# Optimization experiments

Measured on AMD Instinct MI355X. Metric: run time of the kernel, lower is better.

Reference implementation:

```python
import jax, jax.numpy as jnp
import numpy as np

INPUT_DIM = 784
LATENT_DIM = 32
HIDDEN = 256
NUM_PROTO = 25  # 5x5 SOM grid
BATCH = 65536


def setup_inputs() -> dict:
    key = jax.random.key(0)
    ks = jax.random.split(key, 10)
    s = lambda fan_in: 1.0 / np.sqrt(fan_in)
    return {
        "x": jax.random.uniform(ks[0], (BATCH, INPUT_DIM), dtype=jnp.float32),
        # encoder: Linear(784,256) -> ReLU -> Linear(256,32)
        "We1": jax.random.normal(ks[1], (INPUT_DIM, HIDDEN), dtype=jnp.float32) * s(INPUT_DIM),
        "be1": jnp.zeros((HIDDEN,), dtype=jnp.float32),
        "We2": jax.random.normal(ks[2], (HIDDEN, LATENT_DIM), dtype=jnp.float32) * s(HIDDEN),
        "be2": jnp.zeros((LATENT_DIM,), dtype=jnp.float32),
        # decoder: Linear(32,256) -> ReLU -> Linear(256,784) -> Sigmoid
        "Wd1": jax.random.normal(ks[3], (LATENT_DIM, HIDDEN), dtype=jnp.float32) * s(LATENT_DIM),
        "bd1": jnp.zeros((HIDDEN,), dtype=jnp.float32),
        "Wd2": jax.random.normal(ks[4], (HIDDEN, INPUT_DIM), dtype=jnp.float32) * s(HIDDEN),
        "bd2": jnp.zeros((INPUT_DIM,), dtype=jnp.float32),
        # SOM prototypes (torch.randn init)
        "prototypes": jax.random.normal(ks[5], (NUM_PROTO, LATENT_DIM), dtype=jnp.float32),
    }


def reference(x, We1, be1, We2, be2, Wd1, bd1, Wd2, bd2, prototypes):
    # encoder
    h = jax.nn.relu(x @ We1 + be1)          # [B, 256]
    z = h @ We2 + be2                        # [B, 32]
    # SOM layer: cdist -> argmin -> gather winning prototype
    # squared euclidean distance suffices for argmin
    sq_dists = (jnp.sum(z * z, axis=1, keepdims=True)
                - 2.0 * (z @ prototypes.T)
                + jnp.sum(prototypes * prototypes, axis=1))  # [B, 25]
    min_idx = jnp.argmin(sq_dists, axis=1)   # [B]
    som_z = prototypes[min_idx]              # [B, 32]
    # decoder
    hd = jax.nn.relu(som_z @ Wd1 + bd1)      # [B, 256]
    x_recon = jax.nn.sigmoid(hd @ Wd2 + bd2)  # [B, 784]
    return (x_recon, z, som_z)
```

## Files before the change

### kernel.cpp

```cpp
#include <hip/hip_runtime.h>
#include <hip/hip_bf16.h>
#include <math.h>

#define BATCH   65536
#define IN_DIM  784
#define HID     256
#define LAT     32
#define NPROTO  25

typedef short  short8  __attribute__((ext_vector_type(8)));
typedef float  floatx4 __attribute__((ext_vector_type(4)));

__device__ __forceinline__ unsigned short f2bf(float v) {
    __hip_bfloat16 b = __float2bfloat16(v);
    return *reinterpret_cast<unsigned short*>(&b);
}
__device__ __forceinline__ float bf2f(unsigned short u) {
    __hip_bfloat16 b = *reinterpret_cast<__hip_bfloat16*>(&u);
    return __bfloat162float(b);
}
__device__ __forceinline__ void split3(float v, unsigned short& o1,
                                       unsigned short& o2, unsigned short& o3) {
    o1 = f2bf(v); float r1 = v - bf2f(o1);
    o2 = f2bf(r1); float r2 = r1 - bf2f(o2);
    o3 = f2bf(r2);
}

__device__ __forceinline__ floatx4 mm_bf16(short8 a, short8 b, floatx4 c) {
    return __builtin_amdgcn_mfma_f32_16x16x32_bf16(a, b, c, 0, 0, 0);
}

#define BT_SHORTS  204800
#define WS_NEEDED  1307200

__global__ __launch_bounds__(256)
void prep_BF(const float* __restrict__ We1,
             unsigned short* __restrict__ B1,
             unsigned short* __restrict__ B2,
             unsigned short* __restrict__ B3)
{
    int t   = blockIdx.x * 256 + threadIdx.x;
    int l15 = t & 15;
    int q   = (t >> 4) & 3;
    int sn  = t >> 6;
    int s   = sn >> 4;
    int n   = (sn & 15) * 16 + l15;
    int k0  = s * 32 + q * 8;
    short8 v1, v2, v3;
#pragma unroll
    for (int j = 0; j < 8; ++j) {
        int k = k0 + j;
        float v = (k < IN_DIM) ? We1[(size_t)k * HID + n] : 0.f;
        unsigned short a, b, c;
        split3(v, a, b, c);
        v1[j] = (short)a;
        v2[j] = (short)b;
        v3[j] = (short)c;
    }
    size_t o = (size_t)t * 8;
    *(short8*)(B1 + o) = v1;
    *(short8*)(B2 + o) = v2;
    *(short8*)(B3 + o) = v3;
}

__global__ __launch_bounds__(256)
void dpsom_dectab(const float* __restrict__ protos,
                  const float* __restrict__ Wd1,
                  const float* __restrict__ bd1,
                  const float* __restrict__ Wd2,
                  const float* __restrict__ bd2,
                  float* __restrict__ table)
{
    __shared__ float pr[LAT];
    __shared__ float hd[HID];
    const int p = blockIdx.x;
    const int tid = threadIdx.x;
    if (tid < LAT) pr[tid] = protos[p * LAT + tid];
    __syncthreads();
    float s = bd1[tid];
#pragma unroll
    for (int k = 0; k < LAT; ++k)
        s = fmaf(pr[k], Wd1[k * HID + tid], s);
    hd[tid] = fmaxf(s, 0.f);
    __syncthreads();
    for (int i = tid; i < IN_DIM; i += 256) {
        float o = bd2[i];
        for (int j = 0; j < HID; ++j)
            o = fmaf(hd[j], Wd2[(size_t)j * IN_DIM + i], o);
        table[p * IN_DIM + i] = 1.f / (1.f + expf(-o));
    }
}

#define AST  80
#define ABUF 15360

__device__ __forceinline__ void cvt_write3(float4 v0, float4 v1, char* wp) {
    float vv[8] = {v0.x, v0.y, v0.z, v0.w, v1.x, v1.y, v1.z, v1.w};
    short8 u1, u2, u3;
#pragma unroll
    for (int j = 0; j < 8; ++j) {
        unsigned short a, b, c;
        split3(vv[j], a, b, c);
        u1[j] = (short)a;
        u2[j] = (short)b;
        u3[j] = (short)c;
    }
    *(short8*)(wp)          = u1;
    *(short8*)(wp + 5120)   = u2;
    *(short8*)(wp + 10240)  = u3;
}

__global__ __launch_bounds__(256, 3)
void dpsom_encoder_bf3(const float* __restrict__ x,
                       const unsigned short* __restrict__ B1g,
                       const unsigned short* __restrict__ B2g,
                       const unsigned short* __restrict__ B3g,
                       const float* __restrict__ be1,
                       const float* __restrict__ We2,
                       const float* __restrict__ be2,
                       const float* __restrict__ protos,
                       const float* __restrict__ table,
                       float* __restrict__ z_out,
                       float* __restrict__ somz_out,
                       float* __restrict__ xrec)
{
    __shared__ __align__(16) char smem[45056];
    const int tid  = threadIdx.x;
    const int wave = tid >> 6;
    const int lane = tid & 63;
    const int l15  = lane & 15;
    const int q    = lane >> 4;
    const int row0 = blockIdx.x * 64;

    const int arow = tid >> 2;
    const int aq   = tid & 3;
    const float* xrow = x + (size_t)(row0 + arow) * IN_DIM + aq * 8;
    char* awp = smem + arow * AST + aq * 16;

    floatx4 acc[4][4];
#pragma unroll
    for (int i = 0; i < 4; ++i)
#pragma unroll
        for (int j = 0; j < 4; ++j) acc[i][j] = (floatx4)0.f;

    {
        float4 v0 = *(const float4*)(xrow);
        float4 v1 = *(const float4*)(xrow + 4);
        cvt_write3(v0, v1, awp);
    }
    __syncthreads();

    for (int s = 0; s < 25; ++s) {
        const char* abase = smem + (s & 1) * ABUF;
        const int fb = (s * 16 + wave * 4) << 9;

        short8 b1, b2, b3;
        {
            int off0 = fb + (lane << 3);
            b1 = *(const short8*)(B1g + off0);
            b2 = *(const short8*)(B2g + off0);
            b3 = *(const short8*)(B3g + off0);
        }

        float4 v0 = make_float4(0.f, 0.f, 0.f, 0.f), v1 = v0;
        if (s < 24) {
            if ((s < 23) | (aq < 2)) {
                v0 = *(const float4*)(xrow + (s + 1) * 32);
                v1 = *(const float4*)(xrow + (s + 1) * 32 + 4);
            }
        }

        short8 a1f[4], a2f[4], a3f[4];
#pragma unroll
        for (int mf = 0; mf < 4; ++mf) {
            const char* ap = abase + (mf * 16 + l15) * AST + q * 16;
            a1f[mf] = *(const short8*)ap;
            a2f[mf] = *(const short8*)(ap + 5120);
            a3f[mf] = *(const short8*)(ap + 10240);
        }

        if (s < 24) cvt_write3(v0, v1, awp + ((s + 1) & 1) * ABUF);

#pragma unroll
        for (int nf = 0; nf < 4; ++nf) {
            short8 cb1 = b1, cb2 = b2, cb3 = b3;
            if (nf < 3) {
                int offn = fb + ((nf + 1) << 9) + (lane << 3);
                b1 = *(const short8*)(B1g + offn);
                b2 = *(const short8*)(B2g + offn);
                b3 = *(const short8*)(B3g + offn);
            }
#pragma unroll
            for (int mf = 0; mf < 4; ++mf) acc[mf][nf] = mm_bf16(a1f[mf], cb1, acc[mf][nf]);
#pragma unroll
            for (int mf = 0; mf < 4; ++mf) acc[mf][nf] = mm_bf16(a1f[mf], cb2, acc[mf][nf]);
#pragma unroll
            for (int mf = 0; mf < 4; ++mf) acc[mf][nf] = mm_bf16(a2f[mf], cb1, acc[mf][nf]);
#pragma unroll
            for (int mf = 0; mf < 4; ++mf) acc[mf][nf] = mm_bf16(a1f[mf], cb3, acc[mf][nf]);
#pragma unroll
            for (int mf = 0; mf < 4; ++mf) acc[mf][nf] = mm_bf16(a3f[mf], cb1, acc[mf][nf]);
#pragma unroll
            for (int mf = 0; mf < 4; ++mf) acc[mf][nf] = mm_bf16(a2f[mf], cb2, acc[mf][nf]);
        }
        __syncthreads();
    }

    {
        float bias[4];
#pragma unroll
        for (int nf = 0; nf < 4; ++nf) bias[nf] = be1[wave * 64 + 16 * nf + l15];
#pragma unroll
        for (int mf = 0; mf < 4; ++mf)
#pragma unroll
            for (int nf = 0; nf < 4; ++nf)
#pragma unroll
                for (int r = 0; r < 4; ++r)
                    acc[mf][nf][r] = fmaxf(acc[mf][nf][r] + bias[nf], 0.f);
    }

    float* h_lds  = (float*)smem;
    float* z_lds  = (float*)(smem + 33280);
    float* cdist  = (float*)(smem + 41728);
    int*   cidx   = (int*)  (smem + 42752);
    int*   minidx = (int*)  (smem + 43776);

    const int jz = tid & 31;
    const int rg = tid >> 5;
    const float bz = be2[jz];

    for (int hf = 0; hf < 2; ++hf) {
        __syncthreads();
#pragma unroll
        for (int mm = 0; mm < 2; ++mm) {
            int mf = 2 * hf + mm;
#pragma unroll
            for (int nf = 0; nf < 4; ++nf)
#pragma unroll
                for (int r = 0; r < 4; ++r) {
                    int lr = 16 * mm + 4 * q + r;
                    h_lds[lr * 260 + wave * 64 + 16 * nf + l15] = acc[mf][nf][r];
                }
        }
        __syncthreads();
        float s0 = bz, s1 = bz, s2 = bz, s3 = bz;
        const float* h0p = h_lds + (rg * 4 + 0) * 260;
        const float* h1p = h_lds + (rg * 4 + 1) * 260;
        const float* h2p = h_lds + (rg * 4 + 2) * 260;
        const float* h3p = h_lds + (rg * 4 + 3) * 260;
#pragma unroll 4
        for (int c = 0; c < HID; c += 4) {
            float w0 = We2[(c + 0) * LAT + jz];
            float w1 = We2[(c + 1) * LAT + jz];
            float w2 = We2[(c + 2) * LAT + jz];
            float w3 = We2[(c + 3) * LAT + jz];
            float4 h0 = *(const float4*)(h0p + c);
            float4 h1 = *(const float4*)(h1p + c);
            float4 h2 = *(const float4*)(h2p + c);
            float4 h3 = *(const float4*)(h3p + c);
            s0 = fmaf(h0.x, w0, fmaf(h0.y, w1, fmaf(h0.z, w2, fmaf(h0.w, w3, s0))));
            s1 = fmaf(h1.x, w0, fmaf(h1.y, w1, fmaf(h1.z, w2, fmaf(h1.w, w3, s1))));
            s2 = fmaf(h2.x, w0, fmaf(h2.y, w1, fmaf(h2.z, w2, fmaf(h2.w, w3, s2))));
            s3 = fmaf(h3.x, w0, fmaf(h3.y, w1, fmaf(h3.z, w2, fmaf(h3.w, w3, s3))));
        }
        int rbase = hf * 32 + rg * 4;
        z_lds[(rbase + 0) * 33 + jz] = s0;
        z_lds[(rbase + 1) * 33 + jz] = s1;
        z_lds[(rbase + 2) * 33 + jz] = s2;
        z_lds[(rbase + 3) * 33 + jz] = s3;
        z_out[(size_t)(row0 + rbase + 0) * LAT + jz] = s0;
        z_out[(size_t)(row0 + rbase + 1) * LAT + jz] = s1;
        z_out[(size_t)(row0 + rbase + 2) * LAT + jz] = s2;
        z_out[(size_t)(row0 + rbase + 3) * LAT + jz] = s3;
    }
    __syncthreads();

    {
        const int r = tid & 63;
        const int g = tid >> 6;
        float zr[LAT];
        float zn = 0.f;
#pragma unroll
        for (int j = 0; j < LAT; ++j) {
            zr[j] = z_lds[r * 33 + j];
            zn = fmaf(zr[j], zr[j], zn);
        }
        const int p0 = (g == 0) ? 0 : (1 + g * 6);
        const int pc = (g == 0) ? 7 : 6;
        float best = 3.4e38f;
        int bp = p0;
        for (int pi = 0; pi < pc; ++pi) {
            int p = p0 + pi;
            float dot = 0.f, pn = 0.f;
#pragma unroll
            for (int j = 0; j < LAT; ++j) {
                float pv = protos[p * LAT + j];
                dot = fmaf(zr[j], pv, dot);
                pn  = fmaf(pv, pv, pn);
            }
            float d = zn - 2.f * dot + pn;
            if (d < best) { best = d; bp = p; }
        }
        cdist[r * 4 + g] = best;
        cidx[r * 4 + g]  = bp;
    }
    __syncthreads();
    if (tid < 64) {
        float best = cdist[tid * 4];
        int bp = cidx[tid * 4];
#pragma unroll
        for (int g = 1; g < 4; ++g) {
            float d = cdist[tid * 4 + g];
            if (d < best) { best = d; bp = cidx[tid * 4 + g]; }
        }
        minidx[tid] = bp;
    }
    __syncthreads();

#pragma unroll
    for (int m = 0; m < 8; ++m) {
        int r = rg * 8 + m;
        somz_out[(size_t)(row0 + r) * LAT + jz] = protos[minidx[r] * LAT + jz];
    }

    for (int i2 = tid; i2 < 64 * 196; i2 += 256) {
        int row = i2 / 196;
        int c   = i2 - row * 196;
        int idx = minidx[row];
        ((float4*)xrec)[(size_t)(row0 + row) * 196 + c] =
            ((const float4*)table)[idx * 196 + c];
    }
}

#define BMf 64
#define BKf 16
#define HSTRIDE 260
#define ZSTRIDE 33
#define SMEM_FLOATS 10432

__global__ __launch_bounds__(256)
void dpsom_encoder_fp32(const float* __restrict__ x,
                        const float* __restrict__ We1,
                        const float* __restrict__ be1,
                        const float* __restrict__ We2,
                        const float* __restrict__ be2,
                        const float* __restrict__ protos,
                        float* __restrict__ z_out,
                        float* __restrict__ somz_out,
                        int* __restrict__ minidx_out)
{
    __shared__ float smem[SMEM_FLOATS];
    __shared__ int minidx_lds[BMf];
    float* As = smem;
    float* Bs = smem + BKf * BMf;
    float* h_lds = smem;
    float* z_lds = smem + 32 * HSTRIDE;

    const int tid = threadIdx.x;
    const int tx = tid & 31;
    const int ty = tid >> 5;
    const int row0 = blockIdx.x * BMf;

    float acc[8][8];
#pragma unroll
    for (int i = 0; i < 8; ++i)
#pragma unroll
        for (int j = 0; j < 8; ++j) acc[i][j] = 0.f;

    const int ar  = tid >> 2;
    const int akq = tid & 3;

    for (int k0 = 0; k0 < IN_DIM; k0 += BKf) {
        __syncthreads();
        float4 av = *(const float4*)(x + (size_t)(row0 + ar) * IN_DIM + k0 + akq * 4);
        As[(akq * 4 + 0) * BMf + ar] = av.x;
        As[(akq * 4 + 1) * BMf + ar] = av.y;
        As[(akq * 4 + 2) * BMf + ar] = av.z;
        As[(akq * 4 + 3) * BMf + ar] = av.w;
#pragma unroll
        for (int i = 0; i < 4; ++i) {
            int f  = tid + i * 256;
            int bk = f >> 6;
            int bn = (f & 63) << 2;
            *(float4*)(Bs + bk * HID + bn) =
                *(const float4*)(We1 + (size_t)(k0 + bk) * HID + bn);
        }
        __syncthreads();
#pragma unroll
        for (int kk = 0; kk < BKf; ++kk) {
            float4 a0 = *(const float4*)(As + kk * BMf + ty * 8);
            float4 a1 = *(const float4*)(As + kk * BMf + ty * 8 + 4);
            float4 b0 = *(const float4*)(Bs + kk * HID + tx * 8);
            float4 b1 = *(const float4*)(Bs + kk * HID + tx * 8 + 4);
            float a[8] = {a0.x, a0.y, a0.z, a0.w, a1.x, a1.y, a1.z, a1.w};
            float b[8] = {b0.x, b0.y, b0.z, b0.w, b1.x, b1.y, b1.z, b1.w};
#pragma unroll
            for (int i = 0; i < 8; ++i)
#pragma unroll
                for (int j = 0; j < 8; ++j)
                    acc[i][j] = fmaf(a[i], b[j], acc[i][j]);
        }
    }
    {
        float bias[8];
#pragma unroll
        for (int j = 0; j < 8; ++j) bias[j] = be1[tx * 8 + j];
#pragma unroll
        for (int i = 0; i < 8; ++i)
#pragma unroll
            for (int j = 0; j < 8; ++j)
                acc[i][j] = fmaxf(acc[i][j] + bias[j], 0.f);
    }
    const int jz = tid & 31;
    const int rg = tid >> 5;
    const float bz = be2[jz];
    for (int hf = 0; hf < 2; ++hf) {
        __syncthreads();
        if ((ty >> 2) == hf) {
            int rb = (ty & 3) * 8;
#pragma unroll
            for (int i = 0; i < 8; ++i) {
                *(float4*)(h_lds + (rb + i) * HSTRIDE + tx * 8) =
                    make_float4(acc[i][0], acc[i][1], acc[i][2], acc[i][3]);
                *(float4*)(h_lds + (rb + i) * HSTRIDE + tx * 8 + 4) =
                    make_float4(acc[i][4], acc[i][5], acc[i][6], acc[i][7]);
            }
        }
        __syncthreads();
        float s0 = bz, s1 = bz, s2 = bz, s3 = bz;
        const float* h0p = h_lds + (rg * 4 + 0) * HSTRIDE;
        const float* h1p = h_lds + (rg * 4 + 1) * HSTRIDE;
        const float* h2p = h_lds + (rg * 4 + 2) * HSTRIDE;
        const float* h3p = h_lds + (rg * 4 + 3) * HSTRIDE;
#pragma unroll 4
        for (int c = 0; c < HID; c += 4) {
            float w0 = We2[(c + 0) * LAT + jz];
            float w1 = We2[(c + 1) * LAT + jz];
            float w2 = We2[(c + 2) * LAT + jz];
            float w3 = We2[(c + 3) * LAT + jz];
            float4 h0 = *(const float4*)(h0p + c);
            float4 h1 = *(const float4*)(h1p + c);
            float4 h2 = *(const float4*)(h2p + c);
            float4 h3 = *(const float4*)(h3p + c);
            s0 = fmaf(h0.x, w0, fmaf(h0.y, w1, fmaf(h0.z, w2, fmaf(h0.w, w3, s0))));
            s1 = fmaf(h1.x, w0, fmaf(h1.y, w1, fmaf(h1.z, w2, fmaf(h1.w, w3, s1))));
            s2 = fmaf(h2.x, w0, fmaf(h2.y, w1, fmaf(h2.z, w2, fmaf(h2.w, w3, s2))));
            s3 = fmaf(h3.x, w0, fmaf(h3.y, w1, fmaf(h3.z, w2, fmaf(h3.w, w3, s3))));
        }
        int rbase = hf * 32 + rg * 4;
        z_lds[(rbase + 0) * ZSTRIDE + jz] = s0;
        z_lds[(rbase + 1) * ZSTRIDE + jz] = s1;
        z_lds[(rbase + 2) * ZSTRIDE + jz] = s2;
        z_lds[(rbase + 3) * ZSTRIDE + jz] = s3;
        z_out[(size_t)(row0 + rbase + 0) * LAT + jz] = s0;
        z_out[(size_t)(row0 + rbase + 1) * LAT + jz] = s1;
        z_out[(size_t)(row0 + rbase + 2) * LAT + jz] = s2;
        z_out[(size_t)(row0 + rbase + 3) * LAT + jz] = s3;
    }
    __syncthreads();
    if (tid < BMf) {
        float zr[LAT];
        float zn = 0.f;
#pragma unroll
        for (int j = 0; j < LAT; ++j) {
            zr[j] = z_lds[tid * ZSTRIDE + j];
            zn = fmaf(zr[j], zr[j], zn);
        }
        float best = 3.4e38f;
        int bp = 0;
        for (int p = 0; p < NPROTO; ++p) {
            float dot = 0.f, pn = 0.f;
#pragma unroll
            for (int j = 0; j < LAT; ++j) {
                float pv = protos[p * LAT + j];
                dot = fmaf(zr[j], pv, dot);
                pn  = fmaf(pv, pv, pn);
            }
            float d = zn - 2.f * dot + pn;
            if (d < best) { best = d; bp = p; }
        }
        minidx_out[row0 + tid] = bp;
        minidx_lds[tid] = bp;
    }
    __syncthreads();
#pragma unroll
    for (int m = 0; m < 8; ++m) {
        int r = rg * 8 + m;
        somz_out[(size_t)(row0 + r) * LAT + jz] = protos[minidx_lds[r] * LAT + jz];
    }
}

__global__ __launch_bounds__(256)
void dpsom_gather(const float4* __restrict__ table,
                  const int* __restrict__ minidx,
                  float4* __restrict__ xrec)
{
    const int f = blockIdx.x * 256 + threadIdx.x;
    const int row = f / 196;
    const int c4  = f - row * 196;
    const int idx = minidx[row];
    xrec[f] = table[idx * 196 + c4];
}

extern "C" void kernel_launch(void* const* d_in, const int* in_sizes, int n_in,
                              void* d_out, int out_size, void* d_ws, size_t ws_size,
                              hipStream_t stream)
{
    const float* x    = (const float*)d_in[0];
    const float* We1  = (const float*)d_in[1];
    const float* be1  = (const float*)d_in[2];
    const float* We2  = (const float*)d_in[3];
    const float* be2  = (const float*)d_in[4];
    const float* Wd1  = (const float*)d_in[5];
    const float* bd1  = (const float*)d_in[6];
    const float* Wd2  = (const float*)d_in[7];
    const float* bd2  = (const float*)d_in[8];
    const float* prot = (const float*)d_in[9];

    float* out   = (float*)d_out;
    float* xrec  = out;
    float* z_out = out + (size_t)BATCH * IN_DIM;
    float* somz  = z_out + (size_t)BATCH * LAT;

    if (ws_size >= WS_NEEDED) {
        unsigned short* B1 = (unsigned short*)d_ws;
        unsigned short* B2 = B1 + BT_SHORTS;
        unsigned short* B3 = B2 + BT_SHORTS;
        float* table = (float*)((char*)d_ws + 1228800);

        hipLaunchKernelGGL(prep_BF, dim3(100), dim3(256), 0, stream, We1, B1, B2, B3);
        hipLaunchKernelGGL(dpsom_dectab, dim3(NPROTO), dim3(256), 0, stream,
                           prot, Wd1, bd1, Wd2, bd2, table);
        hipLaunchKernelGGL(dpsom_encoder_bf3, dim3(BATCH / 64), dim3(256), 0, stream,
                           x, B1, B2, B3, be1, We2, be2, prot, table,
                           z_out, somz, xrec);
    } else {
        int*   minidx = (int*)d_ws;
        float* table  = (float*)((char*)d_ws + (size_t)BATCH * 4);
        hipLaunchKernelGGL(dpsom_encoder_fp32, dim3(BATCH / BMf), dim3(256), 0, stream,
                           x, We1, be1, We2, be2, prot, z_out, somz, minidx);
        hipLaunchKernelGGL(dpsom_dectab, dim3(NPROTO), dim3(256), 0, stream,
                           prot, Wd1, bd1, Wd2, bd2, table);
        hipLaunchKernelGGL(dpsom_gather, dim3((BATCH * (IN_DIM / 4)) / 256), dim3(256), 0, stream,
                           (const float4*)table, minidx, (float4*)xrec);
    }
}
```

Measured before the change: 527.3 us.

## Prefetch whole next k-step of B fragments and swizzle A LDS layout

The encoder main loop now loads all four B fragments (three bf16 splits each) for the next k-step into a second register set, ping-ponging between two register buffers across an unrolled pair of steps. Previously it prefetched only one fragment ahead inside the step. The A tile in LDS switches from a padded 80-byte row stride to a dense 64-byte stride with an XOR swizzle, shrinking the buffer and aiming to avoid bank conflicts. The A conversion store is moved after the MFMAs. This doubles the B register footprint (24 extra short8), which risks spills or lower occupancy under the launch_bounds(256,3) constraint.

```diff
diff --git a/kernel.cpp b/kernel.cpp
--- a/kernel.cpp
+++ b/kernel.cpp
@@ -91,8 +91,8 @@
     }
 }
 
-#define AST  80
-#define ABUF 15360
+#define AARR 4096
+#define ABUF 12288
 
 __device__ __forceinline__ void cvt_write3(float4 v0, float4 v1, char* wp) {
     float vv[8] = {v0.x, v0.y, v0.z, v0.w, v1.x, v1.y, v1.z, v1.w};
@@ -105,9 +105,9 @@
         u2[j] = (short)b;
         u3[j] = (short)c;
     }
-    *(short8*)(wp)          = u1;
-    *(short8*)(wp + 5120)   = u2;
-    *(short8*)(wp + 10240)  = u3;
+    *(short8*)(wp)            = u1;
+    *(short8*)(wp + AARR)     = u2;
+    *(short8*)(wp + 2 * AARR) = u3;
 }
 
 __global__ __launch_bounds__(256, 3)
@@ -130,38 +130,51 @@
     const int lane = tid & 63;
     const int l15  = lane & 15;
     const int q    = lane >> 4;
+    const int sw   = (l15 >> 1) & 3;
     const int row0 = blockIdx.x * 64;
 
     const int arow = tid >> 2;
     const int aq   = tid & 3;
+    const int awoff = arow * 64 + (aq ^ ((arow >> 1) & 3)) * 16;
     const float* xrow = x + (size_t)(row0 + arow) * IN_DIM + aq * 8;
-    char* awp = smem + arow * AST + aq * 16;
 
     floatx4 acc[4][4];
 #pragma unroll
     for (int i = 0; i < 4; ++i)
 #pragma unroll
         for (int j = 0; j < 4; ++j) acc[i][j] = (floatx4)0.f;
+
+    short8 bA1[4], bA2[4], bA3[4];
+    short8 bB1[4], bB2[4], bB3[4];
 
     {
         float4 v0 = *(const float4*)(xrow);
         float4 v1 = *(const float4*)(xrow + 4);
-        cvt_write3(v0, v1, awp);
-    }
-    __syncthreads();
-
-    for (int s = 0; s < 25; ++s) {
-        const char* abase = smem + (s & 1) * ABUF;
-        const int fb = (s * 16 + wave * 4) << 9;
-
-        short8 b1, b2, b3;
-        {
-            int off0 = fb + (lane << 3);
-            b1 = *(const short8*)(B1g + off0);
-            b2 = *(const short8*)(B2g + off0);
-            b3 = *(const short8*)(B3g + off0);
-        }
-
+        cvt_write3(v0, v1, smem + awoff);
+        const int fb = (wave * 4) << 9;
+#pragma unroll
+        for (int nf = 0; nf < 4; ++nf) {
+            int off = fb + (nf << 9) + (lane << 3);
+            bA1[nf] = *(const short8*)(B1g + off);
+            bA2[nf] = *(const short8*)(B2g + off);
+            bA3[nf] = *(const short8*)(B3g + off);
+        }
+    }
+    __syncthreads();
+
+    auto kstep = [&](int s,
+                     short8 (&c1)[4], short8 (&c2)[4], short8 (&c3)[4],
+                     short8 (&n1)[4], short8 (&n2)[4], short8 (&n3)[4]) {
+        if (s < 24) {
+            const int fb = ((s + 1) * 16 + wave * 4) << 9;
+#pragma unroll
+            for (int nf = 0; nf < 4; ++nf) {
+                int off = fb + (nf << 9) + (lane << 3);
+                n1[nf] = *(const short8*)(B1g + off);
+                n2[nf] = *(const short8*)(B2g + off);
+                n3[nf] = *(const short8*)(B3g + off);
+            }
+        }
         float4 v0 = make_float4(0.f, 0.f, 0.f, 0.f), v1 = v0;
         if (s < 24) {
             if ((s < 23) | (aq < 2)) {
@@ -169,42 +182,39 @@
                 v1 = *(const float4*)(xrow + (s + 1) * 32 + 4);
             }
         }
-
+        const char* abase = smem + (s & 1) * ABUF;
         short8 a1f[4], a2f[4], a3f[4];
 #pragma unroll
         for (int mf = 0; mf < 4; ++mf) {
-            const char* ap = abase + (mf * 16 + l15) * AST + q * 16;
+            const char* ap = abase + (16 * mf + l15) * 64 + ((q ^ sw) * 16);
             a1f[mf] = *(const short8*)ap;
-            a2f[mf] = *(const short8*)(ap + 5120);
-            a3f[mf] = *(const short8*)(ap + 10240);
-        }
-
-        if (s < 24) cvt_write3(v0, v1, awp + ((s + 1) & 1) * ABUF);
-
+            a2f[mf] = *(const short8*)(ap + AARR);
+            a3f[mf] = *(const short8*)(ap + 2 * AARR);
+        }
 #pragma unroll
         for (int nf = 0; nf < 4; ++nf) {
-            short8 cb1 = b1, cb2 = b2, cb3 = b3;
-            if (nf < 3) {
-                int offn = fb + ((nf + 1) << 9) + (lane << 3);
-                b1 = *(const short8*)(B1g + offn);
-                b2 = *(const short8*)(B2g + offn);
-                b3 = *(const short8*)(B3g + offn);
-            }
-#pragma unroll
-            for (int mf = 0; mf < 4; ++mf) acc[mf][nf] = mm_bf16(a1f[mf], cb1, acc[mf][nf]);
-#pragma unroll
-            for (int mf = 0; mf < 4; ++mf) acc[mf][nf] = mm_bf16(a1f[mf], cb2, acc[mf][nf]);
-#pragma unroll
-            for (int mf = 0; mf < 4; ++mf) acc[mf][nf] = mm_bf16(a2f[mf], cb1, acc[mf][nf]);
-#pragma unroll
-            for (int mf = 0; mf < 4; ++mf) acc[mf][nf] = mm_bf16(a1f[mf], cb3, acc[mf][nf]);
-#pragma unroll
-            for (int mf = 0; mf < 4; ++mf) acc[mf][nf] = mm_bf16(a3f[mf], cb1, acc[mf][nf]);
-#pragma unroll
-            for (int mf = 0; mf < 4; ++mf) acc[mf][nf] = mm_bf16(a2f[mf], cb2, acc[mf][nf]);
-        }
-        __syncthreads();
-    }
+#pragma unroll
+            for (int mf = 0; mf < 4; ++mf) acc[mf][nf] = mm_bf16(a1f[mf], c1[nf], acc[mf][nf]);
+#pragma unroll
+            for (int mf = 0; mf < 4; ++mf) acc[mf][nf] = mm_bf16(a1f[mf], c2[nf], acc[mf][nf]);
+#pragma unroll
+            for (int mf = 0; mf < 4; ++mf) acc[mf][nf] = mm_bf16(a2f[mf], c1[nf], acc[mf][nf]);
+#pragma unroll
+            for (int mf = 0; mf < 4; ++mf) acc[mf][nf] = mm_bf16(a1f[mf], c3[nf], acc[mf][nf]);
+#pragma unroll
+            for (int mf = 0; mf < 4; ++mf) acc[mf][nf] = mm_bf16(a3f[mf], c1[nf], acc[mf][nf]);
+#pragma unroll
+            for (int mf = 0; mf < 4; ++mf) acc[mf][nf] = mm_bf16(a2f[mf], c2[nf], acc[mf][nf]);
+        }
+        if (s < 24) cvt_write3(v0, v1, smem + ((s + 1) & 1) * ABUF + awoff);
+        __syncthreads();
+    };
+
+    for (int sp = 0; sp < 12; ++sp) {
+        kstep(2 * sp,     bA1, bA2, bA3, bB1, bB2, bB3);
+        kstep(2 * sp + 1, bB1, bB2, bB3, bA1, bA2, bA3);
+    }
+    kstep(24, bA1, bA2, bA3, bB1, bB2, bB3);
 
     {
         float bias[4];
```

Measured after the change: 910.5 us. 1.73x slower.
